# Performance work log

Measured on AMD Instinct MI355X. Metric: run time of the kernel, lower is better.

## Reference

```python
import jax, jax.numpy as jnp
import numpy as np

T, D_IN, D_OUT = 8192, 1024, 1024
TRACE, CONTEXT = 64, 16


def setup_inputs() -> dict:
    key = jax.random.key(0)
    ks = jax.random.split(key, 8)
    x = jax.random.normal(ks[0], (T, D_IN), jnp.float32)
    state_re = jnp.zeros((1, TRACE, CONTEXT), jnp.float32)
    state_im = jnp.zeros((1, TRACE, CONTEXT), jnp.float32)
    start = jax.random.bernoulli(ks[1], 0.01, (T,))
    next_done = jax.random.bernoulli(ks[2], 0.01, (T,))
    lim_in = 1.0 / np.sqrt(D_IN)
    W_pre = jax.random.uniform(ks[3], (TRACE, D_IN), jnp.float32, -lim_in, lim_in)
    b_pre = jnp.zeros((TRACE,), jnp.float32)
    W_skip = jax.random.uniform(ks[4], (D_OUT, D_IN), jnp.float32, -lim_in, lim_in)
    b_skip = jnp.zeros((D_OUT,), jnp.float32)
    d_mix = 2 * TRACE * CONTEXT
    lim_mix = 1.0 / np.sqrt(d_mix)
    W_mix = jax.random.uniform(ks[5], (D_OUT, d_mix), jnp.float32, -lim_mix, lim_mix)
    b_mix = jnp.zeros((D_OUT,), jnp.float32)
    # ffa.init: deterministic decay rates a and oscillation freqs b (FFM paper)
    a = jnp.linspace(1e-6, 0.5, TRACE)
    b_freq = 2.0 * jnp.pi / jnp.linspace(1.0, 1024.0, CONTEXT)
    return dict(x=x, state_re=state_re, state_im=state_im, start=start, next_done=next_done,
                W_pre=W_pre, b_pre=b_pre, W_skip=W_skip, b_skip=b_skip,
                W_mix=W_mix, b_mix=b_mix, a=a, b_freq=b_freq)


def _ffa_scan(pre, state0, start, a, b_freq):
    """Resettable complex linear recurrence: S_t = gamma * S_{t-1} * !start_t + pre_t.
    pre: [T, m] real, state0: [1, m, c] complex. Returns [T, m, c] complex."""
    n = pre.shape[0]
    ab = (-jnp.abs(a)[:, None] + 1j * b_freq[None, :]).astype(jnp.complex64)  # [m, c]
    x_c = jnp.broadcast_to(pre[:, :, None], (n, pre.shape[1], b_freq.shape[0])).astype(jnp.complex64)
    # prepend carried-in state as an extra element with no decay (t=0) and no reset
    x_c = jnp.concatenate([state0, x_c], axis=0)
    s = jnp.concatenate([jnp.zeros((1,), bool), start.astype(bool)], axis=0)
    t = jnp.concatenate([jnp.zeros((1,), jnp.float32), jnp.ones((n,), jnp.float32)], axis=0)

    def combine(l, r):
        sl, xl, tl = l
        sr, xr, tr = r
        keep = jnp.logical_not(sr)  # right segment starts an episode -> drop left
        decay = jnp.exp(ab[None, :, :] * tr[:, None, None])  # gamma^{t_right}
        x = jnp.where(keep[:, None, None], xl * decay, jnp.zeros((), jnp.complex64)) + xr
        return (jnp.logical_or(sl, sr), x, tl * keep + tr)

    _, states, _ = jax.lax.associative_scan(combine, (s, x_c, t), axis=0)
    return states[1:]


def reference(x, state_re, state_im, start, next_done,
              W_pre, b_pre, W_skip, b_skip, W_mix, b_mix, a, b_freq):
    pre = x @ W_pre.T + b_pre                                  # [T, m]
    pre = pre / (1e-6 + jnp.linalg.norm(pre, axis=-1, keepdims=True))
    state0 = (state_re + 1j * state_im).astype(jnp.complex64)   # [1, m, c]
    states = _ffa_scan(pre, state0, start, a, b_freq)           # [T, m, c] complex
    z_in = jnp.concatenate([jnp.real(states), jnp.imag(states)], axis=-1)
    z_in = z_in.reshape(states.shape[0], -1)                    # [T, 2*m*c]
    z = z_in @ W_mix.T + b_mix                                  # [T, d_out]
    skip = x @ W_skip.T + b_skip                                # [T, d_out]
    return (z + skip, states[-1:])
```

## Files before the change

### kernel.cpp

```cpp
#include <hip/hip_runtime.h>
#include <hip/hip_bf16.h>
#include <stdint.h>

#define T_LEN 8192
#define DIN   1024
#define DOUT  1024
#define TRACE 64
#define CTX   16
#define KTOT  3072
#define CH    64
#define NCHUNK 128

#define AS1 __attribute__((address_space(1)))
#define AS3 __attribute__((address_space(3)))

#define BAR() asm volatile("s_barrier" ::: "memory")

using bf16 = __hip_bfloat16;
typedef __attribute__((ext_vector_type(4))) float f32x4;
typedef __attribute__((ext_vector_type(8))) short s16x8;

__device__ __forceinline__ void pack4(const float4 v, void* dst) {
    union { bf16 h[4]; uint2 u; } pk;
    pk.h[0] = __float2bfloat16(v.x); pk.h[1] = __float2bfloat16(v.y);
    pk.h[2] = __float2bfloat16(v.z); pk.h[3] = __float2bfloat16(v.w);
    *(uint2*)dst = pk.u;
}

__global__ void cvt_x(const float* __restrict__ x, const float* __restrict__ Wpre,
                      bf16* __restrict__ A, bf16* __restrict__ Wp) {
    int idx = blockIdx.x * 256 + threadIdx.x;
    if (idx < 2097152) {
        int r = idx >> 8, c4 = (idx & 255) << 2;
        pack4(*(const float4*)(x + (size_t)r * 1024 + c4), A + (size_t)r * KTOT + c4);
    } else if (idx < 2113536) {
        int i = idx - 2097152;
        int r = i >> 8, c4 = (i & 255) << 2;
        pack4(*(const float4*)(Wpre + (size_t)r * 1024 + c4), Wp + (size_t)r * 1024 + c4);
    }
}

__global__ __launch_bounds__(256) void pre_scan1(
    const bf16* __restrict__ A,
    const bf16* __restrict__ Wp,
    const float* __restrict__ bpre,
    const int* __restrict__ start,
    const float* __restrict__ a, const float* __restrict__ bfreq,
    float* __restrict__ pre_raw,
    float2* __restrict__ local_end,
    int* __restrict__ reset_any) {
    __shared__ short As[2][64 * 32];
    __shared__ short Bs[2][64 * 32];
    __shared__ float pn[CH][TRACE + 1];
    __shared__ float rn[CH];
    __shared__ int sf[CH];
    const int tid = threadIdx.x, lane = tid & 63, wv = tid >> 6;
    const int row0 = blockIdx.x * 64;
    const int l4 = lane >> 2, c8 = (lane & 3) * 8;

    auto stage = [&](int kt, int buf) {
        int r = wv * 16 + l4;
        const bf16* ga = A + (size_t)(row0 + r) * KTOT + kt * 32 + c8;
        const bf16* gb = Wp + (size_t)r * 1024 + kt * 32 + c8;
        __builtin_amdgcn_global_load_lds(
            (const AS1 void*)ga, (AS3 void*)&As[buf][wv * 512], 16, 0, 0);
        __builtin_amdgcn_global_load_lds(
            (const AS1 void*)gb, (AS3 void*)&Bs[buf][wv * 512], 16, 0, 0);
    };

    f32x4 acc[4];
#pragma unroll
    for (int j = 0; j < 4; ++j) acc[j] = (f32x4)0.0f;

    stage(0, 0);
    __syncthreads();
    int buf = 0;
    const int lr = lane & 15, lk = (lane >> 4) * 8;
    for (int kt = 0; kt < 32; ++kt) {
        if (kt + 1 < 32) stage(kt + 1, buf ^ 1);
        s16x8 af = *(const s16x8*)&As[buf][(wv * 16 + lr) * 32 + lk];
        s16x8 bfr[4];
#pragma unroll
        for (int j = 0; j < 4; ++j)
            bfr[j] = *(const s16x8*)&Bs[buf][(j * 16 + lr) * 32 + lk];
#pragma unroll
        for (int j = 0; j < 4; ++j)
            acc[j] = __builtin_amdgcn_mfma_f32_16x16x32_bf16(af, bfr[j], acc[j], 0, 0, 0);
        __syncthreads();
        buf ^= 1;
    }
    const int lg = lane >> 4;
#pragma unroll
    for (int j = 0; j < 4; ++j) {
        int col = j * 16 + lr;
        float bias = bpre[col];
#pragma unroll
        for (int r = 0; r < 4; ++r) {
            int rl = wv * 16 + lg * 4 + r;
            float v = acc[j][r] + bias;
            pn[rl][col] = v;
            pre_raw[(size_t)(row0 + rl) * TRACE + col] = v;
        }
    }
    if (tid < CH) sf[tid] = start[row0 + tid];
    __syncthreads();
    if (tid < CH) {
        float s = 0.f;
#pragma unroll
        for (int m = 0; m < TRACE; ++m) { float v = pn[tid][m]; s += v * v; }
        rn[tid] = 1.0f / (1e-6f + sqrtf(s));
        int any = __any(sf[tid] != 0);
        if (tid == 0) reset_any[blockIdx.x] = any;
    }
    __syncthreads();
#pragma unroll
    for (int q = 0; q < 4; ++q) {
        int pair = tid + q * 256;
        int m = pair >> 4, c = pair & 15;
        float am = a[m], th = bfreq[c];
        float e = expf(-fabsf(am));
        float sn, cs; sincosf(th, &sn, &cs);
        float gr = e * cs, gi = e * sn;
        float sre = 0.f, sim = 0.f;
        for (int r = 0; r < CH; ++r) {
            float p = pn[r][m] * rn[r];
            if (sf[r]) { sre = p; sim = 0.f; }
            else { float t = gr * sre - gi * sim + p; sim = gr * sim + gi * sre; sre = t; }
        }
        local_end[(size_t)blockIdx.x * 1024 + pair] = make_float2(sre, sim);
    }
}

__global__ void scan_phase2w(const float2* __restrict__ local_end, const int* __restrict__ reset_any,
                             const float* __restrict__ state_re, const float* __restrict__ state_im,
                             const float* __restrict__ a, const float* __restrict__ bfreq,
                             float2* __restrict__ carry_in, float* __restrict__ out_tail, int tail_n,
                             const float* __restrict__ Wsk, const float* __restrict__ Wmx,
                             bf16* __restrict__ Bc) {
    if (blockIdx.x >= 16) {
        int idx = (blockIdx.x - 16) * 256 + threadIdx.x;
        if (idx < 262144) {
            int r = idx >> 8, c4 = (idx & 255) << 2;
            pack4(*(const float4*)(Wsk + (size_t)r * 1024 + c4), Bc + (size_t)r * KTOT + c4);
        } else {
            int i = idx - 262144;
            int r = i >> 9, c4 = (i & 511) << 2;
            pack4(*(const float4*)(Wmx + (size_t)r * 2048 + c4), Bc + (size_t)r * KTOT + 1024 + c4);
        }
        return;
    }
    if (threadIdx.x >= 64) return;
    const int pair = blockIdx.x * 64 + threadIdx.x;
    const int m = pair >> 4, c = pair & 15;
    float am = a[m], th = bfreq[c];
    float e = expf(-64.f * fabsf(am));
    float sn, cs; sincosf(64.f * th, &sn, &cs);
    float gr = e * cs, gi = e * sn;
    float cre = state_re[pair], cim = state_im[pair];

    float2 pf[8]; int rsv[8];
#pragma unroll
    for (int j = 0; j < 8; ++j) { pf[j] = local_end[(size_t)j * 1024 + pair]; rsv[j] = reset_any[j]; }
    for (int kb = 0; kb < NCHUNK; kb += 8) {
        float2 cur[8]; int rs[8];
#pragma unroll
        for (int j = 0; j < 8; ++j) { cur[j] = pf[j]; rs[j] = rsv[j]; }
        if (kb + 8 < NCHUNK) {
#pragma unroll
            for (int j = 0; j < 8; ++j) {
                pf[j]  = local_end[(size_t)(kb + 8 + j) * 1024 + pair];
                rsv[j] = reset_any[kb + 8 + j];
            }
        }
#pragma unroll
        for (int j = 0; j < 8; ++j) {
            carry_in[(size_t)(kb + j) * 1024 + pair] = make_float2(cre, cim);
            if (rs[j]) { cre = cur[j].x; cim = cur[j].y; }
            else {
                float t = gr * cre - gi * cim + cur[j].x;
                cim = gr * cim + gi * cre + cur[j].y;
                cre = t;
            }
        }
    }
    if (pair < tail_n)        out_tail[pair]        = cre;
    if (1024 + pair < tail_n) out_tail[1024 + pair] = cim;
}

__global__ void scan_phase3(const float* __restrict__ pre_raw, const int* __restrict__ start,
                            const float* __restrict__ a, const float* __restrict__ bfreq,
                            const float2* __restrict__ carry_in, bf16* __restrict__ A) {
    __shared__ float pn[CH][TRACE + 1];
    __shared__ float rn[CH];
    __shared__ int sf[CH];
    const int k = blockIdx.x >> 1, h = blockIdx.x & 1, tid = threadIdx.x;
    for (int idx = tid; idx < CH * TRACE; idx += 256) {
        int r = idx >> 6, m = idx & 63;
        pn[r][m] = pre_raw[(size_t)(k * CH + r) * TRACE + m];
    }
    if (tid < CH) sf[tid] = start[k * CH + tid];
    __syncthreads();
    if (tid < CH) {
        float s = 0.f;
#pragma unroll
        for (int m = 0; m < TRACE; ++m) { float v = pn[tid][m]; s += v * v; }
        rn[tid] = 1.0f / (1e-6f + sqrtf(s));
    }
    __syncthreads();
    {
        int p0 = h * 512 + tid * 2;
        int m = p0 >> 4, c0 = p0 & 15;
        float am = a[m];
        float e = expf(-fabsf(am));
        float sn0, cs0, sn1, cs1;
        sincosf(bfreq[c0], &sn0, &cs0);
        sincosf(bfreq[c0 + 1], &sn1, &cs1);
        float gr0 = e * cs0, gi0 = e * sn0;
        float gr1 = e * cs1, gi1 = e * sn1;
        float4 ci = *(const float4*)&carry_in[(size_t)k * 1024 + p0];
        float sre0 = ci.x, sim0 = ci.y, sre1 = ci.z, sim1 = ci.w;
        for (int r = 0; r < CH; ++r) {
            float p = pn[r][m] * rn[r];
            if (sf[r]) { sre0 = p; sim0 = 0.f; sre1 = p; sim1 = 0.f; }
            else {
                float t0 = gr0 * sre0 - gi0 * sim0 + p; sim0 = gr0 * sim0 + gi0 * sre0; sre0 = t0;
                float t1 = gr1 * sre1 - gi1 * sim1 + p; sim1 = gr1 * sim1 + gi1 * sre1; sre1 = t1;
            }
            size_t off = (size_t)(k * CH + r) * KTOT + 1024 + m * 32;
            union { bf16 h2[2]; uint32_t u; } pr, pi;
            pr.h2[0] = __float2bfloat16(sre0); pr.h2[1] = __float2bfloat16(sre1);
            pi.h2[0] = __float2bfloat16(sim0); pi.h2[1] = __float2bfloat16(sim1);
            *(uint32_t*)(A + off + c0)      = pr.u;
            *(uint32_t*)(A + off + 16 + c0) = pi.u;
        }
    }
}

__global__ __launch_bounds__(512) void gemm_main(const bf16* __restrict__ A,
                                                 const bf16* __restrict__ B,
                                                 const float* __restrict__ bskip,
                                                 const float* __restrict__ bmix,
                                                 float* __restrict__ out) {
    __shared__ short As[3][256 * 64];
    __shared__ short Bs[3][128 * 64];
    const int tid = threadIdx.x;
    const int lane = tid & 63, wv = tid >> 6;
    const int wm = wv >> 1, wn = wv & 1;
    const int wg = blockIdx.x;
    const int xcd = wg & 7, bidx = wg >> 3;
    const int row0 = (xcd * 4 + (bidx >> 3)) * 256;
    const int col0 = (bidx & 7) * 128;

    const int rl8 = lane >> 3;
    const int u8  = lane & 7;
    const int ksw = (u8 ^ rl8) << 3;

    auto stageBatch = [&](int su, int bd, int sb) {
#pragma unroll
        for (int jj = 0; jj < 2; ++jj) {
            int j = sb * 2 + jj;
            int r = wv * 32 + j * 8 + rl8;
            const bf16* ga = A + (size_t)(row0 + r) * KTOT + su * 64 + ksw;
            __builtin_amdgcn_global_load_lds((const AS1 void*)ga,
                (AS3 void*)&As[bd][(wv * 32 + j * 8) * 64], 16, 0, 0);
        }
        int rb = wv * 16 + sb * 8 + rl8;
        const bf16* gb = B + (size_t)(col0 + rb) * KTOT + su * 64 + ksw;
        __builtin_amdgcn_global_load_lds((const AS1 void*)gb,
            (AS3 void*)&Bs[bd][(wv * 16 + sb * 8) * 64], 16, 0, 0);
    };

    f32x4 acc[4][4];
#pragma unroll
    for (int i = 0; i < 4; ++i)
#pragma unroll
        for (int j = 0; j < 4; ++j) acc[i][j] = (f32x4)0.0f;

    const int lr = lane & 15, hi = lane >> 4;
    const int sw0 = ((0 + hi) ^ (lr & 7)) << 3;
    const int sw1 = ((4 + hi) ^ (lr & 7)) << 3;

    s16x8 af[4][2], bfr[4][2];

    auto phase = [&](int bc, int h, int su, int bd, int vm) {
        if (h == 0) {
#pragma unroll
            for (int i = 0; i < 4; ++i) {
                af[i][0] = *(const s16x8*)&As[bc][(wm * 64 + i * 16 + lr) * 64 + sw0];
                af[i][1] = *(const s16x8*)&As[bc][(wm * 64 + i * 16 + lr) * 64 + sw1];
            }
#pragma unroll
            for (int j = 0; j < 2; ++j) {
                bfr[j][0] = *(const s16x8*)&Bs[bc][(wn * 64 + j * 16 + lr) * 64 + sw0];
                bfr[j][1] = *(const s16x8*)&Bs[bc][(wn * 64 + j * 16 + lr) * 64 + sw1];
            }
        } else {
#pragma unroll
            for (int j = 2; j < 4; ++j) {
                bfr[j][0] = *(const s16x8*)&Bs[bc][(wn * 64 + j * 16 + lr) * 64 + sw0];
                bfr[j][1] = *(const s16x8*)&Bs[bc][(wn * 64 + j * 16 + lr) * 64 + sw1];
            }
        }
        if (su >= 0) stageBatch(su, bd, h);
        BAR();
        __builtin_amdgcn_s_setprio(1);
#pragma unroll
        for (int kk = 0; kk < 2; ++kk)
#pragma unroll
            for (int i = 0; i < 4; ++i)
#pragma unroll
                for (int jj = 0; jj < 2; ++jj) {
                    int j = h * 2 + jj;
                    acc[i][j] = __builtin_amdgcn_mfma_f32_16x16x32_bf16(af[i][kk], bfr[j][kk], acc[i][j], 0, 0, 0);
                }
        __builtin_amdgcn_s_setprio(0);
        if (vm == 6)      asm volatile("s_waitcnt vmcnt(6)" ::: "memory");
        else if (vm == 0) asm volatile("s_waitcnt vmcnt(0)" ::: "memory");
        asm volatile("s_waitcnt lgkmcnt(0)" ::: "memory");
        BAR();
    };

    stageBatch(0, 0, 0); stageBatch(0, 0, 1);
    stageBatch(1, 1, 0); stageBatch(1, 1, 1);
    asm volatile("s_waitcnt vmcnt(6)" ::: "memory");
    BAR();

    for (int t = 0; t < 15; ++t) {
        int u0 = 3 * t;
        phase(0, 0, u0 + 2, 2, -1);
        phase(0, 1, u0 + 2, 2,  6);
        phase(1, 0, u0 + 3, 0, -1);
        phase(1, 1, u0 + 3, 0,  6);
        phase(2, 0, u0 + 4, 1, -1);
        phase(2, 1, u0 + 4, 1,  6);
    }
    phase(0, 0, 47, 2, -1);
    phase(0, 1, 47, 2,  6);
    phase(1, 0, -1, 0, -1);
    phase(1, 1, -1, 0,  0);
    phase(2, 0, -1, 0, -1);
    phase(2, 1, -1, 0, -1);

    const int lg = lane >> 4;
#pragma unroll
    for (int j = 0; j < 4; ++j) {
        int col = col0 + wn * 64 + j * 16 + lr;
        float bias = bskip[col] + bmix[col];
#pragma unroll
        for (int i = 0; i < 4; ++i) {
            int rbase = row0 + wm * 64 + i * 16 + lg * 4;
#pragma unroll
            for (int r = 0; r < 4; ++r)
                out[(size_t)(rbase + r) * DOUT + col] = acc[i][j][r] + bias;
        }
    }
}

extern "C" void kernel_launch(void* const* d_in, const int* in_sizes, int n_in,
                              void* d_out, int out_size, void* d_ws, size_t ws_size,
                              hipStream_t stream) {
    const float* x        = (const float*)d_in[0];
    const float* state_re = (const float*)d_in[1];
    const float* state_im = (const float*)d_in[2];
    const int*   start    = (const int*)d_in[3];
    const float* W_pre    = (const float*)d_in[5];
    const float* b_pre    = (const float*)d_in[6];
    const float* W_skip   = (const float*)d_in[7];
    const float* b_skip   = (const float*)d_in[8];
    const float* W_mix    = (const float*)d_in[9];
    const float* b_mix    = (const float*)d_in[10];
    const float* a_dec    = (const float*)d_in[11];
    const float* b_freq   = (const float*)d_in[12];

    uint8_t* ws = (uint8_t*)d_ws;
    bf16*  A         = (bf16*)(ws);
    bf16*  Bc        = (bf16*)(ws + 50331648);
    bf16*  Wp        = (bf16*)(ws + 56623104);
    float* pre_raw   = (float*)(ws + 56754176);
    float2* local_end= (float2*)(ws + 58851328);
    float2* carry_in = (float2*)(ws + 59899904);
    int*   reset_any = (int*)(ws + 60948480);

    cvt_x<<<dim3((2113536 + 255) / 256), 256, 0, stream>>>(x, W_pre, A, Wp);

    pre_scan1<<<dim3(NCHUNK), 256, 0, stream>>>(A, Wp, b_pre, start, a_dec, b_freq,
                                                pre_raw, local_end, reset_any);
    int tail_n = out_size - 8192 * 1024;
    if (tail_n < 0) tail_n = 0;
    if (tail_n > 2048) tail_n = 2048;
    scan_phase2w<<<dim3(16 + 3072), 256, 0, stream>>>(local_end, reset_any, state_re, state_im,
                                                      a_dec, b_freq, carry_in,
                                                      (float*)d_out + 8192 * 1024, tail_n,
                                                      W_skip, W_mix, Bc);
    scan_phase3<<<dim3(2 * NCHUNK), 256, 0, stream>>>(pre_raw, start, a_dec, b_freq, carry_in, A);

    gemm_main<<<dim3(256), 512, 0, stream>>>(A, Bc, b_skip, b_mix, (float*)d_out);
}
```

Baseline: 119.3 us.

## Shrink GEMM tile to 128x128 with BK=32 and launch twice the blocks

The main bf16 MFMA GEMM moves from 256x128 tiles with 512 threads and a K-step of 64 to 128x128 tiles with 256 threads and a K-step of 32. The grid doubles to 512 blocks, and the staging, LDS swizzle and triple-buffer pipeline are rewritten around a single K phase per buffer. The goal is to cut LDS use per block and raise occupancy and load balance across CUs. The cost is twice as many barriers per unit of K and less operand reuse per tile, so global and LDS traffic per FLOP goes up.

```diff
diff --git a/kernel.cpp b/kernel.cpp
--- a/kernel.cpp
+++ b/kernel.cpp
@@ -236,38 +236,35 @@
     }
 }
 
-__global__ __launch_bounds__(512) void gemm_main(const bf16* __restrict__ A,
+__global__ __launch_bounds__(256) void gemm_main(const bf16* __restrict__ A,
                                                  const bf16* __restrict__ B,
                                                  const float* __restrict__ bskip,
                                                  const float* __restrict__ bmix,
                                                  float* __restrict__ out) {
-    __shared__ short As[3][256 * 64];
-    __shared__ short Bs[3][128 * 64];
+    __shared__ short As[3][128 * 32];
+    __shared__ short Bs[3][128 * 32];
     const int tid = threadIdx.x;
     const int lane = tid & 63, wv = tid >> 6;
     const int wm = wv >> 1, wn = wv & 1;
     const int wg = blockIdx.x;
     const int xcd = wg & 7, bidx = wg >> 3;
-    const int row0 = (xcd * 4 + (bidx >> 3)) * 256;
+    const int row0 = (xcd * 8 + (bidx >> 3)) * 128;
     const int col0 = (bidx & 7) * 128;
 
-    const int rl8 = lane >> 3;
-    const int u8  = lane & 7;
-    const int ksw = (u8 ^ rl8) << 3;
-
-    auto stageBatch = [&](int su, int bd, int sb) {
-#pragma unroll
-        for (int jj = 0; jj < 2; ++jj) {
-            int j = sb * 2 + jj;
-            int r = wv * 32 + j * 8 + rl8;
-            const bf16* ga = A + (size_t)(row0 + r) * KTOT + su * 64 + ksw;
+    const int kswst = ((lane & 3) ^ ((lane >> 3) & 3)) << 3;
+
+    auto stageK = [&](int su, int bd) {
+#pragma unroll
+        for (int j = 0; j < 2; ++j) {
+            int chunk = wv * 2 + j;
+            int r = chunk * 16 + (lane >> 2);
+            const bf16* ga = A + (size_t)(row0 + r) * KTOT + su * 32 + kswst;
             __builtin_amdgcn_global_load_lds((const AS1 void*)ga,
-                (AS3 void*)&As[bd][(wv * 32 + j * 8) * 64], 16, 0, 0);
-        }
-        int rb = wv * 16 + sb * 8 + rl8;
-        const bf16* gb = B + (size_t)(col0 + rb) * KTOT + su * 64 + ksw;
-        __builtin_amdgcn_global_load_lds((const AS1 void*)gb,
-            (AS3 void*)&Bs[bd][(wv * 16 + sb * 8) * 64], 16, 0, 0);
+                (AS3 void*)&As[bd][chunk * 512], 16, 0, 0);
+            const bf16* gb = B + (size_t)(col0 + r) * KTOT + su * 32 + kswst;
+            __builtin_amdgcn_global_load_lds((const AS1 void*)gb,
+                (AS3 void*)&Bs[bd][chunk * 512], 16, 0, 0);
+        }
     };
 
     f32x4 acc[4][4];
@@ -277,69 +274,41 @@
         for (int j = 0; j < 4; ++j) acc[i][j] = (f32x4)0.0f;
 
     const int lr = lane & 15, hi = lane >> 4;
-    const int sw0 = ((0 + hi) ^ (lr & 7)) << 3;
-    const int sw1 = ((4 + hi) ^ (lr & 7)) << 3;
-
-    s16x8 af[4][2], bfr[4][2];
-
-    auto phase = [&](int bc, int h, int su, int bd, int vm) {
-        if (h == 0) {
-#pragma unroll
-            for (int i = 0; i < 4; ++i) {
-                af[i][0] = *(const s16x8*)&As[bc][(wm * 64 + i * 16 + lr) * 64 + sw0];
-                af[i][1] = *(const s16x8*)&As[bc][(wm * 64 + i * 16 + lr) * 64 + sw1];
-            }
-#pragma unroll
-            for (int j = 0; j < 2; ++j) {
-                bfr[j][0] = *(const s16x8*)&Bs[bc][(wn * 64 + j * 16 + lr) * 64 + sw0];
-                bfr[j][1] = *(const s16x8*)&Bs[bc][(wn * 64 + j * 16 + lr) * 64 + sw1];
-            }
-        } else {
-#pragma unroll
-            for (int j = 2; j < 4; ++j) {
-                bfr[j][0] = *(const s16x8*)&Bs[bc][(wn * 64 + j * 16 + lr) * 64 + sw0];
-                bfr[j][1] = *(const s16x8*)&Bs[bc][(wn * 64 + j * 16 + lr) * 64 + sw1];
-            }
-        }
-        if (su >= 0) stageBatch(su, bd, h);
+    const int sw = ((hi ^ ((lr >> 1) & 3)) << 3);
+
+    auto kphase = [&](int bc, int su, int bd, int vm) {
+        s16x8 af[4], bfr[4];
+#pragma unroll
+        for (int i = 0; i < 4; ++i)
+            af[i] = *(const s16x8*)&As[bc][(wm * 64 + i * 16 + lr) * 32 + sw];
+#pragma unroll
+        for (int j = 0; j < 4; ++j)
+            bfr[j] = *(const s16x8*)&Bs[bc][(wn * 64 + j * 16 + lr) * 32 + sw];
+        if (su < 96) stageK(su, bd);
         BAR();
         __builtin_amdgcn_s_setprio(1);
 #pragma unroll
-        for (int kk = 0; kk < 2; ++kk)
-#pragma unroll
-            for (int i = 0; i < 4; ++i)
-#pragma unroll
-                for (int jj = 0; jj < 2; ++jj) {
-                    int j = h * 2 + jj;
-                    acc[i][j] = __builtin_amdgcn_mfma_f32_16x16x32_bf16(af[i][kk], bfr[j][kk], acc[i][j], 0, 0, 0);
-                }
+        for (int i = 0; i < 4; ++i)
+#pragma unroll
+            for (int j = 0; j < 4; ++j)
+                acc[i][j] = __builtin_amdgcn_mfma_f32_16x16x32_bf16(af[i], bfr[j], acc[i][j], 0, 0, 0);
         __builtin_amdgcn_s_setprio(0);
-        if (vm == 6)      asm volatile("s_waitcnt vmcnt(6)" ::: "memory");
-        else if (vm == 0) asm volatile("s_waitcnt vmcnt(0)" ::: "memory");
+        if (vm == 4) asm volatile("s_waitcnt vmcnt(4)" ::: "memory");
+        else         asm volatile("s_waitcnt vmcnt(0)" ::: "memory");
         asm volatile("s_waitcnt lgkmcnt(0)" ::: "memory");
         BAR();
     };
 
-    stageBatch(0, 0, 0); stageBatch(0, 0, 1);
-    stageBatch(1, 1, 0); stageBatch(1, 1, 1);
-    asm volatile("s_waitcnt vmcnt(6)" ::: "memory");
+    stageK(0, 0); stageK(1, 1);
+    asm volatile("s_waitcnt vmcnt(4)" ::: "memory");
     BAR();
 
-    for (int t = 0; t < 15; ++t) {
+    for (int t = 0; t < 32; ++t) {
         int u0 = 3 * t;
-        phase(0, 0, u0 + 2, 2, -1);
-        phase(0, 1, u0 + 2, 2,  6);
-        phase(1, 0, u0 + 3, 0, -1);
-        phase(1, 1, u0 + 3, 0,  6);
-        phase(2, 0, u0 + 4, 1, -1);
-        phase(2, 1, u0 + 4, 1,  6);
-    }
-    phase(0, 0, 47, 2, -1);
-    phase(0, 1, 47, 2,  6);
-    phase(1, 0, -1, 0, -1);
-    phase(1, 1, -1, 0,  0);
-    phase(2, 0, -1, 0, -1);
-    phase(2, 1, -1, 0, -1);
+        kphase(0, u0 + 2, 2, (u0     < 94) ? 4 : 0);
+        kphase(1, u0 + 3, 0, (u0 + 1 < 94) ? 4 : 0);
+        kphase(2, u0 + 4, 1, (u0 + 2 < 94) ? 4 : 0);
+    }
 
     const int lg = lane >> 4;
 #pragma unroll
@@ -394,5 +363,5 @@
                                                       W_skip, W_mix, Bc);
     scan_phase3<<<dim3(2 * NCHUNK), 256, 0, stream>>>(pre_raw, start, a_dec, b_freq, carry_in, A);
 
-    gemm_main<<<dim3(256), 512, 0, stream>>>(A, Bc, b_skip, b_mix, (float*)d_out);
-}
+    gemm_main<<<dim3(512), 256, 0, stream>>>(A, Bc, b_skip, b_mix, (float*)d_out);
+}
```

After: 119.4 us. Within noise of the previous version (+0.1%).
